# Kernel optimization log

Measured on AMD Instinct MI355X. Metric: run time of the kernel, lower is better.

Reference implementation:

```python
import jax, jax.numpy as jnp
import numpy as np

B, J, H, HI, TI, L, D, K = 2048, 23, 512, 512, 64, 4, 512, 2048

def _ln(x, g, b, eps=1e-5):
    m = x.mean(-1, keepdims=True)
    v = ((x - m) ** 2).mean(-1, keepdims=True)
    return (x - m) / jnp.sqrt(v + eps) * g + b

def _mixer(x, ln1, tw1, tb1, tw2, tb2, ln2, cw1, cb1, cw2, cb2):
    # PCT MixerLayer: token-mixing MLP over joint axis, channel MLP over hidden axis
    y = _ln(x, ln1[0], ln1[1]).transpose(0, 2, 1)            # [B, H, J]
    y = jax.nn.gelu(y @ tw1 + tb1, approximate=False) @ tw2 + tb2
    y = y.transpose(0, 2, 1)                                  # [B, J, H]
    z = _ln(x + y, ln2[0], ln2[1])
    z = jax.nn.gelu(z @ cw1 + cb1, approximate=False) @ cw2 + cb2
    return x + y + z

def _forward(pose, start_w, start_b,
             enc_ln1, enc_tw1, enc_tb1, enc_tw2, enc_tb2, enc_ln2,
             enc_cw1, enc_cb1, enc_cw2, enc_cb2, enc_lnf,
             tok_w, tok_b, feat_w, feat_b, codebook,
             dec_tok_w, dec_tok_b, dec_start_w, dec_start_b,
             dec_ln1, dec_tw1, dec_tb1, dec_tw2, dec_tb2, dec_ln2,
             dec_cw1, dec_cb1, dec_cw2, dec_cb2, dec_lnf, rec_w, rec_b):
    bs = pose.shape[0]
    x = pose @ start_w + start_b                               # [B, J, H]
    for i in range(L):
        x = _mixer(x, enc_ln1[i], enc_tw1[i], enc_tb1[i], enc_tw2[i], enc_tb2[i],
                   enc_ln2[i], enc_cw1[i], enc_cb1[i], enc_cw2[i], enc_cb2[i])
    x = _ln(x, enc_lnf[0], enc_lnf[1])
    x = (x.transpose(0, 2, 1) @ tok_w + tok_b).transpose(0, 2, 1)
    e = (x @ feat_w + feat_b).reshape(bs * J, D)               # flatten(0,1)
    # squared euclidean distance to codebook + argmin assignment
    d = (e * e).sum(1, keepdims=True) + (codebook * codebook).sum(1) - 2.0 * (e @ codebook.T)
    idx = jnp.argmin(d, axis=1)                                # [B*J]
    q = jnp.take(codebook, idx, axis=0)                        # == one_hot(idx) @ codebook
    e_latent_loss = jnp.mean((jax.lax.stop_gradient(q) - e) ** 2)
    q_st = e + jax.lax.stop_gradient(q - e)                    # straight-through estimator
    t = q_st.reshape(bs, J, D)
    t = (t.transpose(0, 2, 1) @ dec_tok_w + dec_tok_b).transpose(0, 2, 1)
    y = t @ dec_start_w + dec_start_b
    for i in range(L):
        y = _mixer(y, dec_ln1[i], dec_tw1[i], dec_tb1[i], dec_tw2[i], dec_tb2[i],
                   dec_ln2[i], dec_cw1[i], dec_cb1[i], dec_cw2[i], dec_cb2[i])
    y = _ln(y, dec_lnf[0], dec_lnf[1])
    recovered = y @ rec_w + rec_b                              # [B, J, 9]
    return recovered, idx, e_latent_loss

def _ln_params(n, h):
    return jnp.concatenate([jnp.ones((n, 1, h)), jnp.zeros((n, 1, h))], axis=1).astype(jnp.float32)

def setup_inputs():
    key = jax.random.key(0)
    ks = jax.random.split(key, 12)
    w = lambda k, shape, s=0.02: (jax.random.normal(k, shape) * s).astype(jnp.float32)
    def block(k):
        kk = jax.random.split(k, 4)
        return dict(ln1=_ln_params(L, H), tw1=w(kk[0], (L, J, TI)), tb1=jnp.zeros((L, TI), jnp.float32),
                    tw2=w(kk[1], (L, TI, J)), tb2=jnp.zeros((L, J), jnp.float32), ln2=_ln_params(L, H),
                    cw1=w(kk[2], (L, H, HI)), cb1=jnp.zeros((L, HI), jnp.float32),
                    cw2=w(kk[3], (L, HI, H)), cb2=jnp.zeros((L, H), jnp.float32))
    eb, db = block(ks[8]), block(ks[9])
    return {
        "pose": jax.random.normal(ks[0], (B, J, 9), jnp.float32),
        "start_w": w(ks[1], (9, H)), "start_b": jnp.zeros((H,), jnp.float32),
        "enc_ln1": eb["ln1"], "enc_tw1": eb["tw1"], "enc_tb1": eb["tb1"], "enc_tw2": eb["tw2"], "enc_tb2": eb["tb2"],
        "enc_ln2": eb["ln2"], "enc_cw1": eb["cw1"], "enc_cb1": eb["cb1"], "enc_cw2": eb["cw2"], "enc_cb2": eb["cb2"],
        "enc_lnf": jnp.stack([jnp.ones((H,)), jnp.zeros((H,))]).astype(jnp.float32),
        "tok_w": w(ks[2], (J, J)), "tok_b": jnp.zeros((J,), jnp.float32),
        "feat_w": w(ks[3], (H, D)), "feat_b": jnp.zeros((D,), jnp.float32),
        "codebook": jax.random.normal(ks[4], (K, D), jnp.float32),
        "dec_tok_w": w(ks[5], (J, J)), "dec_tok_b": jnp.zeros((J,), jnp.float32),
        "dec_start_w": w(ks[6], (D, H)), "dec_start_b": jnp.zeros((H,), jnp.float32),
        "dec_ln1": db["ln1"], "dec_tw1": db["tw1"], "dec_tb1": db["tb1"], "dec_tw2": db["tw2"], "dec_tb2": db["tb2"],
        "dec_ln2": db["ln2"], "dec_cw1": db["cw1"], "dec_cb1": db["cb1"], "dec_cw2": db["cw2"], "dec_cb2": db["cb2"],
        "dec_lnf": jnp.stack([jnp.ones((H,)), jnp.zeros((H,))]).astype(jnp.float32),
        "rec_w": w(ks[7], (H, 9)), "rec_b": jnp.zeros((9,), jnp.float32),
    }

def reference(pose, start_w, start_b, enc_ln1, enc_tw1, enc_tb1, enc_tw2, enc_tb2, enc_ln2, enc_cw1, enc_cb1, enc_cw2, enc_cb2, enc_lnf, tok_w, tok_b, feat_w, feat_b, codebook, dec_tok_w, dec_tok_b, dec_start_w, dec_start_b, dec_ln1, dec_tw1, dec_tb1, dec_tw2, dec_tb2, dec_ln2, dec_cw1, dec_cb1, dec_cw2, dec_cb2, dec_lnf, rec_w, rec_b):
    return _forward(pose, start_w, start_b, enc_ln1, enc_tw1, enc_tb1, enc_tw2, enc_tb2, enc_ln2, enc_cw1, enc_cb1, enc_cw2, enc_cb2, enc_lnf, tok_w, tok_b, feat_w, feat_b, codebook, dec_tok_w, dec_tok_b, dec_start_w, dec_start_b, dec_ln1, dec_tw1, dec_tb1, dec_tw2, dec_tb2, dec_ln2, dec_cw1, dec_cb1, dec_cw2, dec_cb2, dec_lnf, rec_w, rec_b)
```

## Files before the change

kernel.cpp:

```cpp
#include <hip/hip_runtime.h>

#define NB 2048
#define NJ 23
#define NH 512
#define LN_EPS 1e-5f
#define RSQRT2 0.70710678118654752440f

typedef __attribute__((ext_vector_type(4))) float f32x4;
typedef __attribute__((ext_vector_type(8))) short s16x8;
typedef __attribute__((ext_vector_type(4))) short s16x4;

__device__ __forceinline__ float gelu_f(float x){ return 0.5f*x*(1.0f+erff(x*RSQRT2)); }
__device__ __forceinline__ float2 f2(float x, float y){ float2 r; r.x=x; r.y=y; return r; }
__device__ __forceinline__ float2 f2s(float x){ return f2(x,x); }
__device__ __forceinline__ float2 fma2s(float s, float2 b, float2 c){ return f2(fmaf(s,b.x,c.x), fmaf(s,b.y,c.y)); }

__device__ __forceinline__ void fma4(float4& a, float s, const float4& v){
  a.x = fmaf(s, v.x, a.x); a.y = fmaf(s, v.y, a.y);
  a.z = fmaf(s, v.z, a.z); a.w = fmaf(s, v.w, a.w);
}

__device__ __forceinline__ short f2bf(float x){
  unsigned u = __float_as_uint(x);
  u = (u + 0x7FFFu + ((u >> 16) & 1u)) >> 16;
  return (short)u;
}

__device__ __forceinline__ void g2l16(float* lds, const float* g){
  __builtin_amdgcn_global_load_lds(
    (const __attribute__((address_space(1))) void*)g,
    (__attribute__((address_space(3))) void*)lds,
    16, 0, 0);
}

__device__ __forceinline__ unsigned long long shfl_xor_u64(unsigned long long v, int m){
  int lo = __shfl_xor((int)(unsigned)(v & 0xffffffffULL), m);
  int hi = __shfl_xor((int)(unsigned)(v >> 32), m);
  return ((unsigned long long)(unsigned)hi << 32) | (unsigned long long)(unsigned)lo;
}

__device__ __forceinline__ void row_stats512(const float* xc, float* Lbuf, float* mrs, int t){
  __syncthreads();
  #pragma unroll
  for (int j=0;j<NJ;j++) Lbuf[j*NH + t] = xc[j];
  __syncthreads();
  int wv = t>>6, lane = t&63;
  for (int r = wv; r < NJ; r += 8){
    const float* row = Lbuf + r*NH;
    float4 v0 = *(const float4*)(row + lane*8);
    float4 v1 = *(const float4*)(row + lane*8 + 4);
    float s = v0.x+v0.y+v0.z+v0.w + v1.x+v1.y+v1.z+v1.w;
    #pragma unroll
    for (int o=32;o;o>>=1) s += __shfl_xor(s, o);
    float m = s * (1.0f/512.0f);
    float d, q = 0.f;
    d=v0.x-m; q+=d*d; d=v0.y-m; q+=d*d; d=v0.z-m; q+=d*d; d=v0.w-m; q+=d*d;
    d=v1.x-m; q+=d*d; d=v1.y-m; q+=d*d; d=v1.z-m; q+=d*d; d=v1.w-m; q+=d*d;
    #pragma unroll
    for (int o=32;o;o>>=1) q += __shfl_xor(q, o);
    if (lane==0){
      mrs[r] = m;
      mrs[NJ+r] = 1.0f / sqrtf(q*(1.0f/512.0f) + LN_EPS);
    }
  }
  __syncthreads();
}

__global__ __launch_bounds__(512) void k_start(
  const float* __restrict__ pose, const float* __restrict__ start_w,
  const float* __restrict__ start_b, float* __restrict__ X)
{
  __shared__ float psm[NJ*9];
  int t = threadIdx.x, b = blockIdx.x;
  if (t < NJ*9) psm[t] = pose[b*NJ*9 + t];
  __syncthreads();
  float wreg[9];
  #pragma unroll
  for (int c=0;c<9;c++) wreg[c] = start_w[c*NH + t];
  float sb = start_b[t];
  #pragma unroll
  for (int j=0;j<NJ;j++){
    float a = sb;
    #pragma unroll
    for (int c=0;c<9;c++) a = fmaf(psm[j*9+c], wreg[c], a);
    X[(size_t)(b*NJ+j)*NH + t] = a;
  }
}

__global__ __launch_bounds__(512, 1) void k_tok(
  float* __restrict__ X, float* __restrict__ Y,
  const float* __restrict__ ln1, const float* __restrict__ tw1, const float* __restrict__ tb1,
  const float* __restrict__ tw2, const float* __restrict__ tb2, const float* __restrict__ ln2)
{
  __shared__ float Lbuf[NJ*NH];
  __shared__ float tw1s[NJ*64];
  __shared__ float tw2sT[NJ*64];
  __shared__ float mrs[2*NJ];
  int t = threadIdx.x, b = blockIdx.x;
  for (int i=t; i<NJ*64; i+=512) tw1s[i] = tw1[i];
  for (int i=t; i<NJ*64; i+=512){ int j = i>>6, c = i&63; tw2sT[i] = tw2[c*NJ + j]; }
  float xc[NJ];
  #pragma unroll
  for (int j=0;j<NJ;j++) xc[j] = X[(size_t)(b*NJ+j)*NH + t];
  row_stats512(xc, Lbuf, mrs, t);
  float g1 = ln1[t], b1 = ln1[NH+t];
  float tn[NJ];
  #pragma unroll
  for (int j=0;j<NJ;j++) tn[j] = fmaf((xc[j]-mrs[j])*mrs[NJ+j], g1, b1);
  float yacc[NJ];
  #pragma unroll
  for (int j=0;j<NJ;j++) yacc[j] = tb2[j];
  for (int c=0;c<64;c+=8){
    float u[8];
    #pragma unroll
    for (int i=0;i<8;i++) u[i] = tb1[c+i];
    #pragma unroll
    for (int j=0;j<NJ;j++){
      float tnj = tn[j];
      float4 w0 = *(const float4*)(tw1s + j*64 + c);
      float4 w1 = *(const float4*)(tw1s + j*64 + c + 4);
      u[0]=fmaf(w0.x,tnj,u[0]); u[1]=fmaf(w0.y,tnj,u[1]); u[2]=fmaf(w0.z,tnj,u[2]); u[3]=fmaf(w0.w,tnj,u[3]);
      u[4]=fmaf(w1.x,tnj,u[4]); u[5]=fmaf(w1.y,tnj,u[5]); u[6]=fmaf(w1.z,tnj,u[6]); u[7]=fmaf(w1.w,tnj,u[7]);
    }
    float gu[8];
    #pragma unroll
    for (int i=0;i<8;i++) gu[i] = gelu_f(u[i]);
    #pragma unroll
    for (int j=0;j<NJ;j++){
      float4 w0 = *(const float4*)(tw2sT + j*64 + c);
      float4 w1 = *(const float4*)(tw2sT + j*64 + c + 4);
      float a = yacc[j];
      a=fmaf(w0.x,gu[0],a); a=fmaf(w0.y,gu[1],a); a=fmaf(w0.z,gu[2],a); a=fmaf(w0.w,gu[3],a);
      a=fmaf(w1.x,gu[4],a); a=fmaf(w1.y,gu[5],a); a=fmaf(w1.z,gu[6],a); a=fmaf(w1.w,gu[7],a);
      yacc[j] = a;
    }
  }
  #pragma unroll
  for (int j=0;j<NJ;j++) xc[j] += yacc[j];
  #pragma unroll
  for (int j=0;j<NJ;j++) X[(size_t)(b*NJ+j)*NH + t] = xc[j];
  row_stats512(xc, Lbuf, mrs, t);
  float g2 = ln2[t], b2 = ln2[NH+t];
  #pragma unroll
  for (int j=0;j<NJ;j++)
    Y[(size_t)(b*NJ+j)*NH + t] = fmaf((xc[j]-mrs[j])*mrs[NJ+j], g2, b2);
}

__global__ __launch_bounds__(512) void k_tokf(
  const float* __restrict__ X, float* __restrict__ Y,
  const float* __restrict__ lnf, const float* __restrict__ tokw, const float* __restrict__ tokb)
{
  __shared__ float Lbuf[NJ*NH];
  __shared__ float mrs[2*NJ];
  __shared__ float tokws[NJ*NJ];
  __shared__ float tokbs[NJ];
  int t = threadIdx.x, b = blockIdx.x;
  for (int i=t; i<NJ*NJ; i+=512) tokws[i] = tokw[i];
  if (t<NJ) tokbs[t] = tokb[t];
  float xc[NJ];
  #pragma unroll
  for (int j=0;j<NJ;j++) xc[j] = X[(size_t)(b*NJ+j)*NH + t];
  row_stats512(xc, Lbuf, mrs, t);
  float gF = lnf[t], bF = lnf[NH+t];
  float xt[NJ];
  #pragma unroll
  for (int j=0;j<NJ;j++) xt[j] = tokbs[j];
  #pragma unroll
  for (int jp=0;jp<NJ;jp++){
    float v = fmaf((xc[jp]-mrs[jp])*mrs[NJ+jp], gF, bF);
    #pragma unroll
    for (int j=0;j<NJ;j++) xt[j] = fmaf(tokws[jp*NJ+j], v, xt[j]);
  }
  #pragma unroll
  for (int j=0;j<NJ;j++) Y[(size_t)(b*NJ+j)*NH + t] = xt[j];
}

__global__ __launch_bounds__(512) void k_dtok(
  const unsigned long long* __restrict__ packed, const float* __restrict__ cb,
  float* __restrict__ Y, const float* __restrict__ tokw, const float* __restrict__ tokb)
{
  __shared__ float tokws[NJ*NJ];
  __shared__ float tokbs[NJ];
  __shared__ int idxs[NJ];
  int t = threadIdx.x, b = blockIdx.x;
  for (int i=t; i<NJ*NJ; i+=512) tokws[i] = tokw[i];
  if (t<NJ){
    tokbs[t] = tokb[t];
    idxs[t]  = (int)(unsigned)(packed[b*NJ + t] & 0xffffffffULL);
  }
  __syncthreads();
  float xt[NJ];
  #pragma unroll
  for (int j=0;j<NJ;j++) xt[j] = tokbs[j];
  #pragma unroll
  for (int jp=0;jp<NJ;jp++){
    float qv = cb[(size_t)idxs[jp]*NH + t];
    #pragma unroll
    for (int j=0;j<NJ;j++) xt[j] = fmaf(tokws[jp*NJ+j], qv, xt[j]);
  }
  #pragma unroll
  for (int j=0;j<NJ;j++) Y[(size_t)(b*NJ+j)*NH + t] = xt[j];
}

#define BK 8
#define ATS 68
template<int OP>
__global__ __launch_bounds__(512) void k_gemm(
  const float* __restrict__ A, const float* __restrict__ W, const float* __restrict__ bias,
  const float* __restrict__ R, float* __restrict__ OUT)
{
  __shared__ float asT[2][BK][ATS];
  __shared__ float wt[2][BK][512];
  int t = threadIdx.x;
  int m0 = blockIdx.x * 64;
  int ct = t & 63;
  int rg = t >> 6;
  int r0 = rg * 8;
  int cLo = ct*4, cHi = 256 + ct*4;
  int lane = t & 63, wv = t >> 6;
  int sar = t >> 3, sak = t & 7;
  const float* Aptr = A + (size_t)(m0+sar)*NH + sak;

  float4 accLo[8], accHi[8];
  #pragma unroll
  for (int i=0;i<8;i++){ accLo[i]=make_float4(0,0,0,0); accHi[i]=make_float4(0,0,0,0); }

  {
    g2l16(&wt[0][wv][0],   W + (size_t)wv*NH + lane*4);
    g2l16(&wt[0][wv][256], W + (size_t)wv*NH + 256 + lane*4);
    asT[0][sak][sar] = *Aptr;
  }
  __syncthreads();

  for (int kt=0; kt<64; ++kt){
    int cur = kt&1, nxt = cur^1;
    float av = 0.f;
    if (kt+1 < 64){
      int kc = (kt+1)*BK;
      av = Aptr[kc];
      g2l16(&wt[nxt][wv][0],   W + (size_t)(kc+wv)*NH + lane*4);
      g2l16(&wt[nxt][wv][256], W + (size_t)(kc+wv)*NH + 256 + lane*4);
    }
    #pragma unroll 2
    for (int k=0;k<BK;k++){
      float4 a0 = *(const float4*)&asT[cur][k][r0];
      float4 a1 = *(const float4*)&asT[cur][k][r0+4];
      float4 w0 = *(const float4*)&wt[cur][k][cLo];
      float4 w1 = *(const float4*)&wt[cur][k][cHi];
      fma4(accLo[0], a0.x, w0); fma4(accHi[0], a0.x, w1);
      fma4(accLo[1], a0.y, w0); fma4(accHi[1], a0.y, w1);
      fma4(accLo[2], a0.z, w0); fma4(accHi[2], a0.z, w1);
      fma4(accLo[3], a0.w, w0); fma4(accHi[3], a0.w, w1);
      fma4(accLo[4], a1.x, w0); fma4(accHi[4], a1.x, w1);
      fma4(accLo[5], a1.y, w0); fma4(accHi[5], a1.y, w1);
      fma4(accLo[6], a1.z, w0); fma4(accHi[6], a1.z, w1);
      fma4(accLo[7], a1.w, w0); fma4(accHi[7], a1.w, w1);
    }
    if (kt+1 < 64) asT[nxt][sak][sar] = av;
    __syncthreads();
  }
  float4 bsLo = *(const float4*)(bias + cLo);
  float4 bsHi = *(const float4*)(bias + cHi);
  #pragma unroll
  for (int i=0;i<8;i++){
    size_t row = (size_t)(m0 + r0 + i);
    float4 v0 = accLo[i], v1 = accHi[i];
    v0.x+=bsLo.x; v0.y+=bsLo.y; v0.z+=bsLo.z; v0.w+=bsLo.w;
    v1.x+=bsHi.x; v1.y+=bsHi.y; v1.z+=bsHi.z; v1.w+=bsHi.w;
    if (OP==0){
      v0.x=gelu_f(v0.x); v0.y=gelu_f(v0.y); v0.z=gelu_f(v0.z); v0.w=gelu_f(v0.w);
      v1.x=gelu_f(v1.x); v1.y=gelu_f(v1.y); v1.z=gelu_f(v1.z); v1.w=gelu_f(v1.w);
    } else if (OP==1){
      float4 r0v = *(const float4*)(R + row*NH + cLo);
      float4 r1v = *(const float4*)(R + row*NH + cHi);
      v0.x+=r0v.x; v0.y+=r0v.y; v0.z+=r0v.z; v0.w+=r0v.w;
      v1.x+=r1v.x; v1.y+=r1v.y; v1.z+=r1v.z; v1.w+=r1v.w;
    }
    *(float4*)(OUT + row*NH + cLo) = v0;
    *(float4*)(OUT + row*NH + cHi) = v1;
  }
}

__global__ __launch_bounds__(512) void k_wsplit(const float* __restrict__ W, short* __restrict__ out){
  int kt = blockIdx.x, t = threadIdx.x;
  int kb = kt*32;
  short* dst = out + (size_t)kt*16384 + (size_t)t*32;
  #pragma unroll 8
  for (int kk=0; kk<32; ++kk)
    dst[kk] = f2bf(W[(size_t)(kb+kk)*NH + t]);
}

#define WPCH 40
template<int OP>
__global__ __launch_bounds__(512) void k_gemm_bfp(
  const float* __restrict__ A, const short* __restrict__ Wpk, const float* __restrict__ bias,
  const float* __restrict__ R, float* __restrict__ OUT)
{
  __shared__ short Wl[512*WPCH];
  __shared__ short Al[64*WPCH];
  int t = threadIdx.x;
  int m0 = blockIdx.x * 64;
  int l = t & 63, w = t >> 6;
  int g = l >> 4, lm = l & 15;
  int ar = t >> 3, ak0 = (t & 7) * 4;

  f32x4 acc[4][4];
  #pragma unroll
  for (int m=0;m<4;m++)
    #pragma unroll
    for (int n=0;n<4;n++){ acc[m][n][0]=0.f; acc[m][n][1]=0.f; acc[m][n][2]=0.f; acc[m][n][3]=0.f; }

  for (int kt=0; kt<16; ++kt){
    __syncthreads();
    const short* src = Wpk + (size_t)kt*16384;
    #pragma unroll
    for (int i=0;i<4;i++){
      int piece = t + i*512;
      s16x8 v = *(const s16x8*)(src + (size_t)piece*8);
      int col = piece >> 2, pc = piece & 3;
      *(s16x8*)&Wl[col*WPCH + pc*8] = v;
    }
    {
      float4 a4 = *(const float4*)(A + (size_t)(m0+ar)*NH + kt*32 + ak0);
      s16x4 v; v[0]=f2bf(a4.x); v[1]=f2bf(a4.y); v[2]=f2bf(a4.z); v[3]=f2bf(a4.w);
      *(s16x4*)&Al[ar*WPCH + ak0] = v;
    }
    __syncthreads();
    s16x8 af0 = *(const s16x8*)&Al[(lm +  0)*WPCH + g*8];
    s16x8 af1 = *(const s16x8*)&Al[(lm + 16)*WPCH + g*8];
    s16x8 af2 = *(const s16x8*)&Al[(lm + 32)*WPCH + g*8];
    s16x8 af3 = *(const s16x8*)&Al[(lm + 48)*WPCH + g*8];
    #pragma unroll
    for (int n=0;n<4;n++){
      int col = w*64 + n*16 + lm;
      s16x8 bfr = *(const s16x8*)&Wl[col*WPCH + g*8];
      acc[0][n] = __builtin_amdgcn_mfma_f32_16x16x32_bf16(af0, bfr, acc[0][n], 0,0,0);
      acc[1][n] = __builtin_amdgcn_mfma_f32_16x16x32_bf16(af1, bfr, acc[1][n], 0,0,0);
      acc[2][n] = __builtin_amdgcn_mfma_f32_16x16x32_bf16(af2, bfr, acc[2][n], 0,0,0);
      acc[3][n] = __builtin_amdgcn_mfma_f32_16x16x32_bf16(af3, bfr, acc[3][n], 0,0,0);
    }
  }
  #pragma unroll
  for (int n=0;n<4;n++){
    int col = w*64 + n*16 + lm;
    float bs = bias[col];
    #pragma unroll
    for (int m=0;m<4;m++){
      #pragma unroll
      for (int r=0;r<4;r++){
        int row = m0 + m*16 + g*4 + r;
        float v = acc[m][n][r] + bs;
        if (OP==0) v = gelu_f(v);
        else if (OP==1) v += R[(size_t)row*NH + col];
        OUT[(size_t)row*NH + col] = v;
      }
    }
  }
}

__global__ void pct_norm_kernel(const float* __restrict__ e, const float* __restrict__ cb,
                                float* __restrict__ enorm, float* __restrict__ cnorm){
  int gw = (blockIdx.x*256 + threadIdx.x)>>6;
  int lane = threadIdx.x & 63;
  int nw = gridDim.x*4;
  for (int r = gw; r < 2048 + 47104; r += nw){
    const float* src = (r < 2048) ? (cb + (size_t)r*512) : (e + (size_t)(r-2048)*512);
    float4 v0 = *(const float4*)(src + lane*8);
    float4 v1 = *(const float4*)(src + lane*8 + 4);
    float q = v0.x*v0.x+v0.y*v0.y+v0.z*v0.z+v0.w*v0.w
            + v1.x*v1.x+v1.y*v1.y+v1.z*v1.z+v1.w*v1.w;
    #pragma unroll
    for (int o=32;o;o>>=1) q += __shfl_xor(q, o);
    if (lane==0){ if (r<2048) cnorm[r]=q; else enorm[r-2048]=q; }
  }
}

#define VBM 64
#define VBN 128
#define VBK 32
#define ETS 68
#define CTS 132
__global__ __launch_bounds__(256, 4) void pct_vq_kernel(
  const float* __restrict__ e, const float* __restrict__ cb,
  const float* __restrict__ enorm, const float* __restrict__ cnorm,
  unsigned long long* __restrict__ packed)
{
  __shared__ float Et[VBK*ETS];
  __shared__ float Ct[VBK*CTS];
  int t = threadIdx.x;
  int row0 = blockIdx.x * VBM;
  int n00  = blockIdx.y * VBN;
  int m0 = (t>>4)<<2;
  int g  = t&15;
  int nA = g*4, nB = 64 + g*4;
  float2 acc[2][8];
  #pragma unroll
  for (int p=0;p<2;p++)
    #pragma unroll
    for (int j=0;j<8;j++) acc[p][j] = f2s(0.f);
  int er = t>>2, eq = t&3;
  int cn = t>>1, ch = t&1;
  for (int kc=0; kc<512; kc+=VBK){
    __syncthreads();
    {
      const float4* src = (const float4*)(e + (size_t)(row0+er)*512 + kc + eq*8);
      float4 a = src[0], bv = src[1];
      float* d0 = Et + (eq*8)*ETS + er;
      d0[0*ETS]=a.x;  d0[1*ETS]=a.y;  d0[2*ETS]=a.z;  d0[3*ETS]=a.w;
      d0[4*ETS]=bv.x; d0[5*ETS]=bv.y; d0[6*ETS]=bv.z; d0[7*ETS]=bv.w;
    }
    {
      const float4* src = (const float4*)(cb + (size_t)(n00+cn)*512 + kc + ch*16);
      float4 a=src[0], b2=src[1], c2=src[2], d2=src[3];
      float* d0 = Ct + (ch*16)*CTS + cn;
      d0[0*CTS]=a.x;   d0[1*CTS]=a.y;   d0[2*CTS]=a.z;   d0[3*CTS]=a.w;
      d0[4*CTS]=b2.x;  d0[5*CTS]=b2.y;  d0[6*CTS]=b2.z;  d0[7*CTS]=b2.w;
      d0[8*CTS]=c2.x;  d0[9*CTS]=c2.y;  d0[10*CTS]=c2.z; d0[11*CTS]=c2.w;
      d0[12*CTS]=d2.x; d0[13*CTS]=d2.y; d0[14*CTS]=d2.z; d0[15*CTS]=d2.w;
    }
    __syncthreads();
    #pragma unroll 8
    for (int k=0;k<VBK;k++){
      float4 av = *(const float4*)(Et + k*ETS + m0);
      float4 b0 = *(const float4*)(Ct + k*CTS + nA);
      float4 b1 = *(const float4*)(Ct + k*CTS + nB);
      float2 a01 = f2(av.x, av.y), a23 = f2(av.z, av.w);
      float bs[8] = {b0.x,b0.y,b0.z,b0.w,b1.x,b1.y,b1.z,b1.w};
      #pragma unroll
      for (int j=0;j<8;j++){
        acc[0][j] = fma2s(bs[j], a01, acc[0][j]);
        acc[1][j] = fma2s(bs[j], a23, acc[1][j]);
      }
    }
  }
  unsigned long long key[4];
  #pragma unroll
  for (int i=0;i<4;i++){
    float en = enorm[row0 + m0 + i];
    unsigned long long kk = ~0ULL;
    #pragma unroll
    for (int j=0;j<8;j++){
      float2 av = acc[i>>1][j];
      float dot = (i&1) ? av.y : av.x;
      int code = n00 + ((j<4) ? (nA + j) : (nB + j - 4));
      float dd = (en + cnorm[code]) - 2.0f*dot;
      unsigned long long kv = ((unsigned long long)__float_as_uint(dd)<<32) | (unsigned long long)(unsigned)code;
      kk = kv < kk ? kv : kk;
    }
    key[i] = kk;
  }
  #pragma unroll
  for (int o=1;o<16;o<<=1){
    #pragma unroll
    for (int i=0;i<4;i++){
      unsigned long long other = shfl_xor_u64(key[i], o);
      key[i] = other < key[i] ? other : key[i];
    }
  }
  if ((t&15)==0){
    #pragma unroll
    for (int i=0;i<4;i++) atomicMin(packed + row0 + m0 + i, key[i]);
  }
}

__global__ void pct_loss_idx_kernel(const float* __restrict__ e, const float* __restrict__ cb,
                                    const unsigned long long* __restrict__ packed,
                                    float* __restrict__ idx_out, float* __restrict__ partials){
  int t = threadIdx.x, lane = t&63;
  int gw = (blockIdx.x*256 + t)>>6;
  int nw = gridDim.x*4;
  float part = 0.f;
  for (int r=gw; r<47104; r+=nw){
    unsigned long long pk = packed[r];
    int idx = (int)(unsigned)(pk & 0xffffffffULL);
    if (lane==0) idx_out[r] = (float)idx;
    const float4* ep = (const float4*)(e + (size_t)r*512);
    const float4* cp = (const float4*)(cb + (size_t)idx*512);
    #pragma unroll
    for (int i=0;i<2;i++){
      float4 ev = ep[lane*2+i], cv = cp[lane*2+i];
      float dx=cv.x-ev.x, dy=cv.y-ev.y, dz=cv.z-ev.z, dw=cv.w-ev.w;
      part += dx*dx+dy*dy+dz*dz+dw*dw;
    }
  }
  #pragma unroll
  for (int o=32;o;o>>=1) part += __shfl_xor(part, o);
  __shared__ float wsum[4];
  if (lane==0) wsum[t>>6] = part;
  __syncthreads();
  if (t==0) partials[blockIdx.x] = wsum[0]+wsum[1]+wsum[2]+wsum[3];
}

__global__ void pct_loss_final_kernel(const float* __restrict__ partials, float* __restrict__ loss){
  float s=0.f;
  for (int i=threadIdx.x; i<256; i+=64) s += partials[i];
  #pragma unroll
  for (int o=32;o;o>>=1) s += __shfl_xor(s, o);
  if (threadIdx.x==0) *loss = s * (1.0f/(47104.0f*512.0f));
}

__global__ __launch_bounds__(512) void k_decfinal(
  const float* __restrict__ X, const float* __restrict__ lnfd,
  const float* __restrict__ rec_w, const float* __restrict__ rec_b,
  float* __restrict__ rec_out)
{
  __shared__ float Lbuf[NJ*NH];
  __shared__ float Ln[NJ*516];
  __shared__ float rws[NH*9];
  __shared__ float mrs[2*NJ];
  int t = threadIdx.x, b = blockIdx.x;
  for (int i=t;i<NH*9;i+=512) rws[i] = rec_w[i];
  float xc[NJ];
  #pragma unroll
  for (int j=0;j<NJ;j++) xc[j] = X[(size_t)(b*NJ+j)*NH + t];
  row_stats512(xc, Lbuf, mrs, t);
  float gF = lnfd[t], bF = lnfd[NH+t];
  #pragma unroll
  for (int j=0;j<NJ;j++)
    Ln[j*516 + t] = fmaf((xc[j]-mrs[j])*mrs[NJ+j], gF, bF);
  __syncthreads();
  if (t < NJ*9){
    int j = t/9, c = t - j*9;
    float a = rec_b[c];
    const float* row = Ln + j*516;
    for (int h=0;h<NH;h++) a = fmaf(row[h], rws[h*9+c], a);
    rec_out[(size_t)(b*NJ+j)*9 + c] = a;
  }
}

extern "C" void kernel_launch(void* const* d_in, const int* in_sizes, int n_in,
                              void* d_out, int out_size, void* d_ws, size_t ws_size,
                              hipStream_t stream) {
  (void)in_sizes; (void)n_in; (void)out_size; (void)ws_size;
  const float* pose        = (const float*)d_in[0];
  const float* start_w     = (const float*)d_in[1];
  const float* start_b     = (const float*)d_in[2];
  const float* enc_ln1     = (const float*)d_in[3];
  const float* enc_tw1     = (const float*)d_in[4];
  const float* enc_tb1     = (const float*)d_in[5];
  const float* enc_tw2     = (const float*)d_in[6];
  const float* enc_tb2     = (const float*)d_in[7];
  const float* enc_ln2     = (const float*)d_in[8];
  const float* enc_cw1     = (const float*)d_in[9];
  const float* enc_cb1     = (const float*)d_in[10];
  const float* enc_cw2     = (const float*)d_in[11];
  const float* enc_cb2     = (const float*)d_in[12];
  const float* enc_lnf     = (const float*)d_in[13];
  const float* tok_w       = (const float*)d_in[14];
  const float* tok_b       = (const float*)d_in[15];
  const float* feat_w      = (const float*)d_in[16];
  const float* feat_b      = (const float*)d_in[17];
  const float* codebook    = (const float*)d_in[18];
  const float* dec_tok_w   = (const float*)d_in[19];
  const float* dec_tok_b   = (const float*)d_in[20];
  const float* dec_start_w = (const float*)d_in[21];
  const float* dec_start_b = (const float*)d_in[22];
  const float* dec_ln1     = (const float*)d_in[23];
  const float* dec_tw1     = (const float*)d_in[24];
  const float* dec_tb1     = (const float*)d_in[25];
  const float* dec_tw2     = (const float*)d_in[26];
  const float* dec_tb2     = (const float*)d_in[27];
  const float* dec_ln2     = (const float*)d_in[28];
  const float* dec_cw1     = (const float*)d_in[29];
  const float* dec_cb1     = (const float*)d_in[30];
  const float* dec_cw2     = (const float*)d_in[31];
  const float* dec_cb2     = (const float*)d_in[32];
  const float* dec_lnf     = (const float*)d_in[33];
  const float* rec_w       = (const float*)d_in[34];
  const float* rec_b       = (const float*)d_in[35];

  const size_t ACT = (size_t)47104*512;
  float* X = (float*)d_ws;
  float* Y = X + ACT;
  unsigned long long* packed = (unsigned long long*)(Y + ACT);
  float* cnorm  = (float*)((char*)packed + (size_t)47104*8);
  float* enormp = cnorm + 2048;
  float* partials = enormp + 47104;
  short* decWpk  = (short*)(partials + 256);

  float* rec_out  = (float*)d_out;
  float* idx_out  = rec_out + 423936;
  float* loss_out = idx_out + 47104;

  (void)hipMemsetAsync(packed, 0xFF, (size_t)47104*8, stream);

  const size_t WSZ = (size_t)512*512;
  k_wsplit<<<16, 512, 0, stream>>>(dec_start_w, decWpk);
  for (int l=0;l<4;l++){
    k_wsplit<<<16, 512, 0, stream>>>(dec_cw1 + l*(NH*NH), decWpk + (1 + 2*l)*WSZ);
    k_wsplit<<<16, 512, 0, stream>>>(dec_cw2 + l*(NH*NH), decWpk + (2 + 2*l)*WSZ);
  }

  k_start<<<NB, 512, 0, stream>>>(pose, start_w, start_b, X);

  const int GG = 736;
  for (int l=0;l<4;l++){
    k_tok<<<NB, 512, 0, stream>>>(X, Y,
      enc_ln1 + l*1024, enc_tw1 + l*(NJ*64), enc_tb1 + l*64,
      enc_tw2 + l*(64*NJ), enc_tb2 + l*NJ, enc_ln2 + l*1024);
    k_gemm<0><<<GG, 512, 0, stream>>>(Y, enc_cw1 + l*(NH*NH), enc_cb1 + l*NH, nullptr, Y);
    k_gemm<1><<<GG, 512, 0, stream>>>(Y, enc_cw2 + l*(NH*NH), enc_cb2 + l*NH, X, X);
  }
  k_tokf<<<NB, 512, 0, stream>>>(X, Y, enc_lnf, tok_w, tok_b);
  k_gemm<2><<<GG, 512, 0, stream>>>(Y, feat_w, feat_b, nullptr, X);

  pct_norm_kernel<<<192, 256, 0, stream>>>(X, codebook, enormp, cnorm);
  pct_vq_kernel<<<dim3(736,16), 256, 0, stream>>>(X, codebook, enormp, cnorm, packed);
  pct_loss_idx_kernel<<<256, 256, 0, stream>>>(X, codebook, packed, idx_out, partials);
  pct_loss_final_kernel<<<1, 64, 0, stream>>>(partials, loss_out);

  k_dtok<<<NB, 512, 0, stream>>>(packed, codebook, Y, dec_tok_w, dec_tok_b);
  k_gemm_bfp<2><<<GG, 512, 0, stream>>>(Y, decWpk, dec_start_b, nullptr, X);

  for (int l=0;l<4;l++){
    k_tok<<<NB, 512, 0, stream>>>(X, Y,
      dec_ln1 + l*1024, dec_tw1 + l*(NJ*64), dec_tb1 + l*64,
      dec_tw2 + l*(64*NJ), dec_tb2 + l*NJ, dec_ln2 + l*1024);
    k_gemm_bfp<0><<<GG, 512, 0, stream>>>(Y, decWpk + (1 + 2*l)*WSZ, dec_cb1 + l*NH, nullptr, Y);
    k_gemm_bfp<1><<<GG, 512, 0, stream>>>(Y, decWpk + (2 + 2*l)*WSZ, dec_cb2 + l*NH, X, X);
  }
  k_decfinal<<<NB, 512, 0, stream>>>(X, dec_lnf, rec_w, rec_b, rec_out);
}
```

Measured before the change: 6.912 ms.

## Widen VQ distance tile to 256 codes with per-wave row blocking

The codebook-distance kernel now covers 256 codes per block instead of 128, which halves the grid in the code dimension. Each wave owns 16 rows and each lane 4 codes, with a 16x4 float4 accumulator per thread. The argmin becomes a full 64-lane shuffle reduction with one atomicMin per row per wave, and the min-waves launch bound is dropped. The aim is to reload the E tile less often and cut atomics, at the cost of more registers, more shared memory and longer shuffle chains.

Result: no change. 6.859 ms (-0.8%).

```diff
diff --git a/kernel.cpp b/kernel.cpp
--- a/kernel.cpp
+++ b/kernel.cpp
@@ -376,11 +376,11 @@
 }
 
 #define VBM 64
-#define VBN 128
+#define VBN 256
 #define VBK 32
 #define ETS 68
-#define CTS 132
-__global__ __launch_bounds__(256, 4) void pct_vq_kernel(
+#define CTS 260
+__global__ __launch_bounds__(256) void pct_vq_kernel(
   const float* __restrict__ e, const float* __restrict__ cb,
   const float* __restrict__ enorm, const float* __restrict__ cnorm,
   unsigned long long* __restrict__ packed)
@@ -390,16 +390,15 @@
   int t = threadIdx.x;
   int row0 = blockIdx.x * VBM;
   int n00  = blockIdx.y * VBN;
-  int m0 = (t>>4)<<2;
-  int g  = t&15;
-  int nA = g*4, nB = 64 + g*4;
-  float2 acc[2][8];
-  #pragma unroll
-  for (int p=0;p<2;p++)
-    #pragma unroll
-    for (int j=0;j<8;j++) acc[p][j] = f2s(0.f);
-  int er = t>>2, eq = t&3;
-  int cn = t>>1, ch = t&1;
+  int w = t >> 6, l = t & 63;
+  int r0 = w * 16;
+  int c0 = l * 4;
+  int er = t >> 2, eq = t & 3;
+
+  float4 acc[16];
+  #pragma unroll
+  for (int i=0;i<16;i++) acc[i] = make_float4(0,0,0,0);
+
   for (int kc=0; kc<512; kc+=VBK){
     __syncthreads();
     {
@@ -410,56 +409,58 @@
       d0[4*ETS]=bv.x; d0[5*ETS]=bv.y; d0[6*ETS]=bv.z; d0[7*ETS]=bv.w;
     }
     {
-      const float4* src = (const float4*)(cb + (size_t)(n00+cn)*512 + kc + ch*16);
-      float4 a=src[0], b2=src[1], c2=src[2], d2=src[3];
-      float* d0 = Ct + (ch*16)*CTS + cn;
-      d0[0*CTS]=a.x;   d0[1*CTS]=a.y;   d0[2*CTS]=a.z;   d0[3*CTS]=a.w;
-      d0[4*CTS]=b2.x;  d0[5*CTS]=b2.y;  d0[6*CTS]=b2.z;  d0[7*CTS]=b2.w;
-      d0[8*CTS]=c2.x;  d0[9*CTS]=c2.y;  d0[10*CTS]=c2.z; d0[11*CTS]=c2.w;
-      d0[12*CTS]=d2.x; d0[13*CTS]=d2.y; d0[14*CTS]=d2.z; d0[15*CTS]=d2.w;
+      const float4* src = (const float4*)(cb + (size_t)(n00+t)*512 + kc);
+      #pragma unroll
+      for (int q=0;q<8;q++){
+        float4 v = src[q];
+        float* d0 = Ct + (q*4)*CTS + t;
+        d0[0*CTS]=v.x; d0[1*CTS]=v.y; d0[2*CTS]=v.z; d0[3*CTS]=v.w;
+      }
     }
     __syncthreads();
-    #pragma unroll 8
+    #pragma unroll 2
     for (int k=0;k<VBK;k++){
-      float4 av = *(const float4*)(Et + k*ETS + m0);
-      float4 b0 = *(const float4*)(Ct + k*CTS + nA);
-      float4 b1 = *(const float4*)(Ct + k*CTS + nB);
-      float2 a01 = f2(av.x, av.y), a23 = f2(av.z, av.w);
-      float bs[8] = {b0.x,b0.y,b0.z,b0.w,b1.x,b1.y,b1.z,b1.w};
-      #pragma unroll
-      for (int j=0;j<8;j++){
-        acc[0][j] = fma2s(bs[j], a01, acc[0][j]);
-        acc[1][j] = fma2s(bs[j], a23, acc[1][j]);
-      }
-    }
-  }
-  unsigned long long key[4];
-  #pragma unroll
-  for (int i=0;i<4;i++){
-    float en = enorm[row0 + m0 + i];
-    unsigned long long kk = ~0ULL;
-    #pragma unroll
-    for (int j=0;j<8;j++){
-      float2 av = acc[i>>1][j];
-      float dot = (i&1) ? av.y : av.x;
-      int code = n00 + ((j<4) ? (nA + j) : (nB + j - 4));
-      float dd = (en + cnorm[code]) - 2.0f*dot;
-      unsigned long long kv = ((unsigned long long)__float_as_uint(dd)<<32) | (unsigned long long)(unsigned)code;
-      kk = kv < kk ? kv : kk;
-    }
-    key[i] = kk;
-  }
-  #pragma unroll
-  for (int o=1;o<16;o<<=1){
-    #pragma unroll
-    for (int i=0;i<4;i++){
-      unsigned long long other = shfl_xor_u64(key[i], o);
-      key[i] = other < key[i] ? other : key[i];
-    }
-  }
-  if ((t&15)==0){
-    #pragma unroll
-    for (int i=0;i<4;i++) atomicMin(packed + row0 + m0 + i, key[i]);
+      const float* ar = &Et[k*ETS + r0];
+      float4 a0 = *(const float4*)(ar);
+      float4 a1 = *(const float4*)(ar + 4);
+      float4 a2 = *(const float4*)(ar + 8);
+      float4 a3 = *(const float4*)(ar + 12);
+      float4 bv = *(const float4*)&Ct[k*CTS + c0];
+      fma4(acc[0],  a0.x, bv); fma4(acc[1],  a0.y, bv);
+      fma4(acc[2],  a0.z, bv); fma4(acc[3],  a0.w, bv);
+      fma4(acc[4],  a1.x, bv); fma4(acc[5],  a1.y, bv);
+      fma4(acc[6],  a1.z, bv); fma4(acc[7],  a1.w, bv);
+      fma4(acc[8],  a2.x, bv); fma4(acc[9],  a2.y, bv);
+      fma4(acc[10], a2.z, bv); fma4(acc[11], a2.w, bv);
+      fma4(acc[12], a3.x, bv); fma4(acc[13], a3.y, bv);
+      fma4(acc[14], a3.z, bv); fma4(acc[15], a3.w, bv);
+    }
+  }
+  float4 cn4 = *(const float4*)(cnorm + n00 + c0);
+  #pragma unroll
+  for (int r=0;r<16;r++){
+    int grow = row0 + r0 + r;
+    float en = enorm[grow];
+    float4 av = acc[r];
+    float d0 = (en + cn4.x) - 2.0f*av.x;
+    float d1 = (en + cn4.y) - 2.0f*av.y;
+    float d2 = (en + cn4.z) - 2.0f*av.z;
+    float d3 = (en + cn4.w) - 2.0f*av.w;
+    int cbase = n00 + c0;
+    unsigned long long kk;
+    kk = ((unsigned long long)__float_as_uint(d0)<<32) | (unsigned long long)(unsigned)(cbase+0);
+    unsigned long long k1 = ((unsigned long long)__float_as_uint(d1)<<32) | (unsigned long long)(unsigned)(cbase+1);
+    unsigned long long k2 = ((unsigned long long)__float_as_uint(d2)<<32) | (unsigned long long)(unsigned)(cbase+2);
+    unsigned long long k3 = ((unsigned long long)__float_as_uint(d3)<<32) | (unsigned long long)(unsigned)(cbase+3);
+    kk = k1 < kk ? k1 : kk;
+    kk = k2 < kk ? k2 : kk;
+    kk = k3 < kk ? k3 : kk;
+    #pragma unroll
+    for (int o=1;o<64;o<<=1){
+      unsigned long long other = shfl_xor_u64(kk, o);
+      kk = other < kk ? other : kk;
+    }
+    if (l==0) atomicMin(packed + grow, kk);
   }
 }
 
@@ -605,7 +606,7 @@
   k_gemm<2><<<GG, 512, 0, stream>>>(Y, feat_w, feat_b, nullptr, X);
 
   pct_norm_kernel<<<192, 256, 0, stream>>>(X, codebook, enormp, cnorm);
-  pct_vq_kernel<<<dim3(736,16), 256, 0, stream>>>(X, codebook, enormp, cnorm, packed);
+  pct_vq_kernel<<<dim3(736,8), 256, 0, stream>>>(X, codebook, enormp, cnorm, packed);
   pct_loss_idx_kernel<<<256, 256, 0, stream>>>(X, codebook, packed, idx_out, partials);
   pct_loss_final_kernel<<<1, 64, 0, stream>>>(partials, loss_out);
 
```
